# Performance work log

Measured on AMD Instinct MI355X. Metric: run time of the kernel, lower is better.

Reference implementation:

```python
import jax, jax.numpy as jnp
import numpy as np

B, D, H = 32768, 688, 4
DH = D // H          # 172 head dim (d_model // h, overrides ctor d_k)
MH = 128             # mlp hidden
EPS = 1e-5
SCALE = 1.0 / float(np.sqrt(DH))


def _ln(x, g, b):
    m = jnp.mean(x, -1, keepdims=True)
    v = jnp.var(x, -1, keepdims=True)  # biased var, matches torch LayerNorm
    return (x - m) / jnp.sqrt(v + EPS) * g + b


def setup_inputs() -> dict:
    key = jax.random.key(0)
    ks = jax.random.split(key, 16)
    w = lambda k, o, i: jax.random.normal(k, (o, i), jnp.float32) * 0.001  # init.normal_(std=0.001)
    z = lambda n: jnp.zeros((n,), jnp.float32)
    o = lambda n: jnp.ones((n,), jnp.float32)
    return dict(
        x=jax.random.normal(ks[0], (B, D), jnp.float32),
        x2=jax.random.normal(ks[1], (B, D), jnp.float32),
        Wq_v=w(ks[2], D, D), bq_v=z(D),
        Wk_v=w(ks[3], D, D), bk_v=z(D),
        Wv_v=w(ks[4], D, D), bv_v=z(D),
        Wq_i=w(ks[5], D, D), bq_i=z(D),
        Wk_i=w(ks[6], D, D), bk_i=z(D),
        Wv_i=w(ks[7], D, D), bv_i=z(D),
        Wo_v=w(ks[8], D, D), bo_v=z(D),
        Wo_i=w(ks[9], D, D), bo_i=z(D),
        ln1_g=o(D), ln1_b=z(D), ln2_g=o(D), ln2_b=z(D),
        ln3_g=o(D), ln3_b=z(D), ln4_g=o(D), ln4_b=z(D),
        m1v_W=w(ks[10], MH, D), m1v_b=z(MH),
        m2v_W=w(ks[11], D, MH), m2v_b=z(D),
        m1i_W=w(ks[12], MH, D), m1i_b=z(MH),
        m2i_W=w(ks[13], D, MH), m2i_b=z(D),
        coef=o(8),  # LearnableCoefficient 1..8, all init to 1.0
    )


def reference(x, x2,
              Wq_v, bq_v, Wk_v, bk_v, Wv_v, bv_v,
              Wq_i, bq_i, Wk_i, bk_i, Wv_i, bv_i,
              Wo_v, bo_v, Wo_i, bo_i,
              ln1_g, ln1_b, ln2_g, ln2_b, ln3_g, ln3_b, ln4_g, ln4_b,
              m1v_W, m1v_b, m2v_W, m2v_b, m1i_W, m1i_b, m2i_W, m2i_b,
              coef):
    rgb = _ln(x, ln1_g, ln1_b)
    ir = _ln(x2, ln2_g, ln2_b)
    proj = lambda t, W, b: (t @ W.T + b).reshape(-1, H, DH)  # (B, h, d_k)
    q_vis, k_vis, v_vis = proj(rgb, Wq_v, bq_v), proj(rgb, Wk_v, bk_v), proj(rgb, Wv_v, bv_v)
    q_ir, k_ir, v_ir = proj(ir, Wq_i, bq_i), proj(ir, Wk_i, bk_i), proj(ir, Wv_i, bv_i)
    # cross attention over heads: scores are (B, h, h)
    att_vis = jax.nn.softmax(jnp.einsum('bhd,bgd->bhg', q_ir, k_vis) * SCALE, -1)
    att_ir = jax.nn.softmax(jnp.einsum('bhd,bgd->bhg', q_vis, k_ir) * SCALE, -1)
    out_vis = jnp.einsum('bhg,bgd->bhd', att_vis, v_vis).reshape(-1, D) @ Wo_v.T + bo_v
    out_ir = jnp.einsum('bhg,bgd->bhd', att_ir, v_ir).reshape(-1, D) @ Wo_i.T + bo_i
    out_vis = coef[0] * x + coef[1] * out_vis
    out_ir = coef[2] * x2 + coef[3] * out_ir
    mv = jax.nn.gelu(_ln(out_vis, ln3_g, ln3_b) @ m1v_W.T + m1v_b, approximate=False) @ m2v_W.T + m2v_b
    mi = jax.nn.gelu(_ln(out_ir, ln4_g, ln4_b) @ m1i_W.T + m1i_b, approximate=False) @ m2i_W.T + m2i_b
    out_vis = coef[4] * out_vis + coef[5] * mv
    out_ir = coef[6] * out_ir + coef[7] * mi
    return out_vis, out_ir
```

## Files before the change

kernel.cpp:

```cpp
#include <hip/hip_runtime.h>
#include <cmath>


#define B_ROWS 32768
#define D_DIM  688
#define DP     704
#define DH_DIM 172
#define MH_DIM 128

typedef unsigned short ushort_t;
typedef __attribute__((ext_vector_type(8))) __bf16 bf16x8;
typedef __attribute__((ext_vector_type(4))) float  f32x4;

__device__ __forceinline__ float b2f(ushort_t u) {
    return __builtin_bit_cast(float, (unsigned int)u << 16);
}
__device__ __forceinline__ ushort_t f2bf(float f) {
    unsigned int u = __builtin_bit_cast(unsigned int, f);
    u += 0x7FFFu + ((u >> 16) & 1u);
    return (ushort_t)(u >> 16);
}

__device__ __forceinline__ void gl2lds16(const ushort_t* g, ushort_t* l) {
    __builtin_amdgcn_global_load_lds(
        (const __attribute__((address_space(1))) unsigned int*)g,
        (__attribute__((address_space(3))) unsigned int*)l, 16, 0, 0);
}

struct CvtJobs {
    const float* src[12];
    ushort_t*    dst[12];
    int O[12], Opad[12], Kin[12], Kpad[12];
    int bstart[13];
};

__global__ __launch_bounds__(256)
void cvt_all(CvtJobs jobs)
{
    int b = blockIdx.x;
    int j = 0;
    while (b >= jobs.bstart[j + 1]) ++j;
    const int t = (b - jobs.bstart[j]) * 256 + threadIdx.x;
    const int Kpad = jobs.Kpad[j];
    const int Kin  = jobs.Kin[j];
    const int cpr  = Kpad >> 3;
    if (t >= jobs.Opad[j] * cpr) return;
    const int o = t / cpr;
    const int c = t - o * cpr;
    unsigned int p0 = 0, p1 = 0, p2 = 0, p3 = 0;
    if (o < jobs.O[j] && (c * 8 + 8) <= Kin) {
        const float* s = jobs.src[j] + (size_t)o * Kin + c * 8;
        float4 f0 = reinterpret_cast<const float4*>(s)[0];
        float4 f1 = reinterpret_cast<const float4*>(s)[1];
        p0 = f2bf(f0.x) | ((unsigned int)f2bf(f0.y) << 16);
        p1 = f2bf(f0.z) | ((unsigned int)f2bf(f0.w) << 16);
        p2 = f2bf(f1.x) | ((unsigned int)f2bf(f1.y) << 16);
        p3 = f2bf(f1.z) | ((unsigned int)f2bf(f1.w) << 16);
    }
    *reinterpret_cast<uint4*>(jobs.dst[j] + (size_t)o * Kpad + c * 8) =
        make_uint4(p0, p1, p2, p3);
}

__global__ __launch_bounds__(256)
void pack_bias(const float* __restrict__ a0, const float* __restrict__ a1,
               const float* __restrict__ a2, const float* __restrict__ b0,
               const float* __restrict__ b1, const float* __restrict__ b2,
               float* __restrict__ dv, float* __restrict__ di)
{
    int t = blockIdx.x * 256 + threadIdx.x;
    if (t >= 2064) return;
    float v, w;
    if (t < 688)       { v = a0[t];        w = b0[t]; }
    else if (t < 1376) { v = a1[t - 688];  w = b1[t - 688]; }
    else               { v = a2[t - 1376]; w = b2[t - 1376]; }
    dv[t] = v; di[t] = w;
}

__global__ __launch_bounds__(256)
void ln_kernel(const float* __restrict__ Xv, const float* __restrict__ Xi,
               const float* __restrict__ gv, const float* __restrict__ bv,
               const float* __restrict__ gi, const float* __restrict__ bi,
               ushort_t* __restrict__ Yv, ushort_t* __restrict__ Yi)
{
    const int lane = threadIdx.x & 63;
    const int wave = threadIdx.x >> 6;
    const long w = (long)blockIdx.x * 4 + wave;
    const float* X; const float* g; const float* b; ushort_t* Y; long r;
    if (w < B_ROWS) { X = Xv; g = gv; b = bv; Y = Yv; r = w; }
    else            { X = Xi; g = gi; b = bi; Y = Yi; r = w - B_ROWS; }

    const float4* row = reinterpret_cast<const float4*>(X + r * D_DIM);
    float4 v0 = row[lane];
    float4 v1 = row[lane + 64];
    float4 v2 = make_float4(0.f, 0.f, 0.f, 0.f);
    if (lane < 44) v2 = row[lane + 128];

    float s  = v0.x + v0.y + v0.z + v0.w + v1.x + v1.y + v1.z + v1.w
             + v2.x + v2.y + v2.z + v2.w;
    float s2 = v0.x*v0.x + v0.y*v0.y + v0.z*v0.z + v0.w*v0.w
             + v1.x*v1.x + v1.y*v1.y + v1.z*v1.z + v1.w*v1.w
             + v2.x*v2.x + v2.y*v2.y + v2.z*v2.z + v2.w*v2.w;
#pragma unroll
    for (int m = 32; m; m >>= 1) { s += __shfl_xor(s, m); s2 += __shfl_xor(s2, m); }

    const float mean = s * (1.f / 688.f);
    const float var  = s2 * (1.f / 688.f) - mean * mean;
    const float rstd = rsqrtf(var + 1e-5f);

    const float4* g4 = reinterpret_cast<const float4*>(g);
    const float4* b4 = reinterpret_cast<const float4*>(b);
    ushort4* out4 = reinterpret_cast<ushort4*>(Y + r * DP);

    {
        float4 gg = g4[lane], bb = b4[lane];
        ushort4 o;
        o.x = f2bf((v0.x - mean) * rstd * gg.x + bb.x);
        o.y = f2bf((v0.y - mean) * rstd * gg.y + bb.y);
        o.z = f2bf((v0.z - mean) * rstd * gg.z + bb.z);
        o.w = f2bf((v0.w - mean) * rstd * gg.w + bb.w);
        out4[lane] = o;
    }
    {
        float4 gg = g4[lane + 64], bb = b4[lane + 64];
        ushort4 o;
        o.x = f2bf((v1.x - mean) * rstd * gg.x + bb.x);
        o.y = f2bf((v1.y - mean) * rstd * gg.y + bb.y);
        o.z = f2bf((v1.z - mean) * rstd * gg.z + bb.z);
        o.w = f2bf((v1.w - mean) * rstd * gg.w + bb.w);
        out4[lane + 64] = o;
    }
    if (lane < 44) {
        float4 gg = g4[lane + 128], bb = b4[lane + 128];
        ushort4 o;
        o.x = f2bf((v2.x - mean) * rstd * gg.x + bb.x);
        o.y = f2bf((v2.y - mean) * rstd * gg.y + bb.y);
        o.z = f2bf((v2.z - mean) * rstd * gg.z + bb.z);
        o.w = f2bf((v2.w - mean) * rstd * gg.w + bb.w);
        out4[lane + 128] = o;
    } else if (lane < 48) {
        out4[lane + 128] = make_ushort4(0, 0, 0, 0);
    }
}

__global__ __launch_bounds__(256)
void ln_bf16(const ushort_t* __restrict__ Xv, const ushort_t* __restrict__ Xi,
             const float* __restrict__ gv, const float* __restrict__ bv,
             const float* __restrict__ gi, const float* __restrict__ bi,
             ushort_t* __restrict__ Yv, ushort_t* __restrict__ Yi)
{
    const int lane = threadIdx.x & 63;
    const int wave = threadIdx.x >> 6;
    const long w = (long)blockIdx.x * 4 + wave;
    const ushort_t* X; const float* g; const float* b; ushort_t* Y; long r;
    if (w < B_ROWS) { X = Xv; g = gv; b = bv; Y = Yv; r = w; }
    else            { X = Xi; g = gi; b = bi; Y = Yi; r = w - B_ROWS; }

    const ushort4* row = reinterpret_cast<const ushort4*>(X + r * D_DIM);
    ushort4 u0 = row[lane];
    ushort4 u1 = row[lane + 64];
    ushort4 u2 = make_ushort4(0, 0, 0, 0);
    if (lane < 44) u2 = row[lane + 128];

    float f0x = b2f(u0.x), f0y = b2f(u0.y), f0z = b2f(u0.z), f0w = b2f(u0.w);
    float f1x = b2f(u1.x), f1y = b2f(u1.y), f1z = b2f(u1.z), f1w = b2f(u1.w);
    float f2x = b2f(u2.x), f2y = b2f(u2.y), f2z = b2f(u2.z), f2w = b2f(u2.w);

    float s  = f0x + f0y + f0z + f0w + f1x + f1y + f1z + f1w + f2x + f2y + f2z + f2w;
    float s2 = f0x*f0x + f0y*f0y + f0z*f0z + f0w*f0w
             + f1x*f1x + f1y*f1y + f1z*f1z + f1w*f1w
             + f2x*f2x + f2y*f2y + f2z*f2z + f2w*f2w;
#pragma unroll
    for (int m = 32; m; m >>= 1) { s += __shfl_xor(s, m); s2 += __shfl_xor(s2, m); }

    const float mean = s * (1.f / 688.f);
    const float var  = s2 * (1.f / 688.f) - mean * mean;
    const float rstd = rsqrtf(var + 1e-5f);

    const float4* g4 = reinterpret_cast<const float4*>(g);
    const float4* b4 = reinterpret_cast<const float4*>(b);
    ushort4* out4 = reinterpret_cast<ushort4*>(Y + r * DP);

    {
        float4 gg = g4[lane], bb = b4[lane];
        ushort4 o;
        o.x = f2bf((f0x - mean) * rstd * gg.x + bb.x);
        o.y = f2bf((f0y - mean) * rstd * gg.y + bb.y);
        o.z = f2bf((f0z - mean) * rstd * gg.z + bb.z);
        o.w = f2bf((f0w - mean) * rstd * gg.w + bb.w);
        out4[lane] = o;
    }
    {
        float4 gg = g4[lane + 64], bb = b4[lane + 64];
        ushort4 o;
        o.x = f2bf((f1x - mean) * rstd * gg.x + bb.x);
        o.y = f2bf((f1y - mean) * rstd * gg.y + bb.y);
        o.z = f2bf((f1z - mean) * rstd * gg.z + bb.z);
        o.w = f2bf((f1w - mean) * rstd * gg.w + bb.w);
        out4[lane + 64] = o;
    }
    if (lane < 44) {
        float4 gg = g4[lane + 128], bb = b4[lane + 128];
        ushort4 o;
        o.x = f2bf((f2x - mean) * rstd * gg.x + bb.x);
        o.y = f2bf((f2y - mean) * rstd * gg.y + bb.y);
        o.z = f2bf((f2z - mean) * rstd * gg.z + bb.z);
        o.w = f2bf((f2w - mean) * rstd * gg.w + bb.w);
        out4[lane + 128] = o;
    } else if (lane < 48) {
        out4[lane + 128] = make_ushort4(0, 0, 0, 0);
    }
}

template<int MODE>
__global__ __launch_bounds__(256, 4)
void gemm2(const ushort_t* __restrict__ A0, const ushort_t* __restrict__ A1,
           const ushort_t* __restrict__ W0, const ushort_t* __restrict__ W1,
           const float* __restrict__ bias0, const float* __restrict__ bias1,
           void* __restrict__ out0, void* __restrict__ out1,
           const void* __restrict__ res0, const void* __restrict__ res1,
           const float* __restrict__ coef,
           int ca0, int cb0, int ca1, int cb1,
           int NBn, int N, int K, int lda, int ldw, int ldo)
{
    __shared__ __align__(16) ushort_t smem[16384];
    ushort_t* As = smem;
    ushort_t* Bs = smem + 8192;

    const int q  = gridDim.x >> 3;
    const int vb = (blockIdx.x & 7) * q + (blockIdx.x >> 3);
    const int nb = vb % NBn;
    const int tmp = vb / NBn;
    const int mb = tmp & 255;
    const int zz = tmp >> 8;

    const ushort_t* A = zz ? A1 : A0;
    const ushort_t* W = zz ? W1 : W0;
    const float* bias = zz ? bias1 : bias0;
    void* outp        = zz ? out1 : out0;
    const void* resid = zz ? res1 : res0;
    const int ca = zz ? ca1 : ca0;
    const int cb = zz ? cb1 : cb0;

    const int tid  = threadIdx.x;
    const int lane = tid & 63;
    const int wave = tid >> 6;
    const int m0 = mb * 128;
    const int n0 = nb * 128;
    const int wm = (wave >> 1) * 64;
    const int wn = (wave & 1) * 64;

    const int s0 = wave * 128 + lane;
    const int s1 = s0 + 64;
    const ushort_t* pa0 = A + (size_t)(m0 + (s0 >> 2)) * lda + (s0 & 3) * 8;
    const ushort_t* pa1 = A + (size_t)(m0 + (s1 >> 2)) * lda + (s1 & 3) * 8;
    const ushort_t* pb0 = W + (size_t)(n0 + (s0 >> 2)) * ldw + (s0 & 3) * 8;
    const ushort_t* pb1 = W + (size_t)(n0 + (s1 >> 2)) * ldw + (s1 & 3) * 8;

    const f32x4 vzero = {0.f, 0.f, 0.f, 0.f};
    f32x4 acc[4][4];
#pragma unroll
    for (int i = 0; i < 4; ++i)
#pragma unroll
        for (int j = 0; j < 4; ++j)
            acc[i][j] = vzero;

    const int ko = (lane >> 4) * 8;
    const int rl = lane & 15;
    const int nkt = K / 32;

    auto stage = [&](int buf, int kt) {
        const int kof = kt * 32;
        ushort_t* ad = As + buf * 4096 + wave * 1024;
        ushort_t* bd = Bs + buf * 4096 + wave * 1024;
        gl2lds16(pa0 + kof, ad);
        gl2lds16(pa1 + kof, ad + 512);
        gl2lds16(pb0 + kof, bd);
        gl2lds16(pb1 + kof, bd + 512);
    };

    stage(0, 0);
    __syncthreads();

    for (int kt = 0; kt < nkt; ++kt) {
        const int cur = kt & 1;
        if (kt + 1 < nkt) stage(cur ^ 1, kt + 1);

        const ushort_t* Ab = As + cur * 4096;
        const ushort_t* Bb = Bs + cur * 4096;
        bf16x8 af[4], bw[4];
#pragma unroll
        for (int i = 0; i < 4; ++i) {
            af[i] = *reinterpret_cast<const bf16x8*>(&Ab[(wm + i * 16 + rl) * 32 + ko]);
            bw[i] = *reinterpret_cast<const bf16x8*>(&Bb[(wn + i * 16 + rl) * 32 + ko]);
        }
#pragma unroll
        for (int i = 0; i < 4; ++i)
#pragma unroll
            for (int j = 0; j < 4; ++j)
                acc[i][j] = __builtin_amdgcn_mfma_f32_16x16x32_bf16(af[i], bw[j], acc[i][j], 0, 0, 0);
        __syncthreads();
    }

    float cA = 0.f, cB = 1.f;
    if constexpr (MODE == 1 || MODE == 3) { cA = coef[ca]; cB = coef[cb]; }
    const int rb = (lane >> 4) * 4;
    const int cl = lane & 15;
    ushort_t* C = smem;
#pragma unroll
    for (int j = 0; j < 4; ++j) {
        const int lcol = wn + j * 16 + cl;
        const int col = n0 + lcol;
        const float bc = (col < N) ? bias[col] : 0.f;
#pragma unroll
        for (int i = 0; i < 4; ++i) {
            const int lrow = wm + i * 16 + rb;
#pragma unroll
            for (int r = 0; r < 4; ++r) {
                float val = acc[i][j][r] + bc;
                if constexpr (MODE == 2)
                    val = 0.5f * val * (1.0f + erff(val * 0.70710678118654752f));
                C[(lrow + r) * 128 + lcol] = f2bf(val);
            }
        }
    }
    __syncthreads();

#pragma unroll
    for (int p = 0; p < 8; ++p) {
        const int c = tid + p * 256;
        const int lrow = c >> 4;
        const int lcl = (c & 15) * 8;
        const int gcol = n0 + lcl;
        if (gcol >= N) continue;
        const size_t idx = (size_t)(m0 + lrow) * ldo + gcol;
        uint4 pv = *reinterpret_cast<const uint4*>(&C[lrow * 128 + lcl]);
        if constexpr (MODE == 0 || MODE == 2) {
            *reinterpret_cast<uint4*>((ushort_t*)outp + idx) = pv;
        } else if constexpr (MODE == 1) {
            const float* rp = (const float*)resid + idx;
            float4 r0 = reinterpret_cast<const float4*>(rp)[0];
            float4 r1 = reinterpret_cast<const float4*>(rp)[1];
            float rr[8] = {r0.x, r0.y, r0.z, r0.w, r1.x, r1.y, r1.z, r1.w};
            const ushort_t* pu = (const ushort_t*)&pv;
            ushort_t o[8];
#pragma unroll
            for (int k = 0; k < 8; ++k)
                o[k] = f2bf(cA * rr[k] + cB * b2f(pu[k]));
            *reinterpret_cast<uint4*>((ushort_t*)outp + idx) = *reinterpret_cast<uint4*>(o);
        } else {
            uint4 rv = *reinterpret_cast<const uint4*>((const ushort_t*)resid + idx);
            const ushort_t* pu = (const ushort_t*)&pv;
            const ushort_t* ru = (const ushort_t*)&rv;
            float o[8];
#pragma unroll
            for (int k = 0; k < 8; ++k)
                o[k] = cA * b2f(ru[k]) + cB * b2f(pu[k]);
            float4* op = reinterpret_cast<float4*>((float*)outp + idx);
            op[0] = make_float4(o[0], o[1], o[2], o[3]);
            op[1] = make_float4(o[4], o[5], o[6], o[7]);
        }
    }
}

__global__ __launch_bounds__(256)
void attn_kernel(const ushort_t* __restrict__ qkv_v, const ushort_t* __restrict__ qkv_i,
                 ushort_t* __restrict__ ctx_v, ushort_t* __restrict__ ctx_i)
{
    const int lane = threadIdx.x & 63;
    const int wave = threadIdx.x >> 6;
    const long r = (long)blockIdx.x * 4 + wave;
    const ushort_t* bv = qkv_v + r * 2064;
    const ushort_t* bi = qkv_i + r * 2064;

    float sv[4][4], si[4][4];
#pragma unroll
    for (int h = 0; h < 4; ++h)
#pragma unroll
        for (int g = 0; g < 4; ++g) { sv[h][g] = 0.f; si[h][g] = 0.f; }

    float vvr[3][4], vir[3][4];
#pragma unroll
    for (int it = 0; it < 3; ++it) {
        const int d = lane + it * 64;
        const bool ok = d < DH_DIM;
        float qv[4], kv[4], qi[4], ki[4];
#pragma unroll
        for (int h = 0; h < 4; ++h) {
            const int o = h * DH_DIM + d;
            qv[h]      = ok ? b2f(bv[o]) : 0.f;
            kv[h]      = ok ? b2f(bv[D_DIM + o]) : 0.f;
            vvr[it][h] = ok ? b2f(bv[2 * D_DIM + o]) : 0.f;
            qi[h]      = ok ? b2f(bi[o]) : 0.f;
            ki[h]      = ok ? b2f(bi[D_DIM + o]) : 0.f;
            vir[it][h] = ok ? b2f(bi[2 * D_DIM + o]) : 0.f;
        }
#pragma unroll
        for (int h = 0; h < 4; ++h)
#pragma unroll
            for (int g = 0; g < 4; ++g) {
                sv[h][g] += qi[h] * kv[g];
                si[h][g] += qv[h] * ki[g];
            }
    }

#pragma unroll
    for (int h = 0; h < 4; ++h)
#pragma unroll
        for (int g = 0; g < 4; ++g) {
            float a = sv[h][g], b = si[h][g];
#pragma unroll
            for (int m = 32; m; m >>= 1) { a += __shfl_xor(a, m); b += __shfl_xor(b, m); }
            sv[h][g] = a; si[h][g] = b;
        }

    const float scale = 0.07624928516630235f;
    float av[4][4], ai[4][4];
#pragma unroll
    for (int h = 0; h < 4; ++h) {
        float m1 = fmaxf(fmaxf(sv[h][0], sv[h][1]), fmaxf(sv[h][2], sv[h][3])) * scale;
        float m2 = fmaxf(fmaxf(si[h][0], si[h][1]), fmaxf(si[h][2], si[h][3])) * scale;
        float d1 = 0.f, d2 = 0.f;
#pragma unroll
        for (int g = 0; g < 4; ++g) {
            av[h][g] = expf(sv[h][g] * scale - m1); d1 += av[h][g];
            ai[h][g] = expf(si[h][g] * scale - m2); d2 += ai[h][g];
        }
        const float r1 = 1.f / d1, r2 = 1.f / d2;
#pragma unroll
        for (int g = 0; g < 4; ++g) { av[h][g] *= r1; ai[h][g] *= r2; }
    }

#pragma unroll
    for (int it = 0; it < 3; ++it) {
        const int d = lane + it * 64;
        if (d < DH_DIM) {
#pragma unroll
            for (int h = 0; h < 4; ++h) {
                float cv = av[h][0] * vvr[it][0] + av[h][1] * vvr[it][1]
                         + av[h][2] * vvr[it][2] + av[h][3] * vvr[it][3];
                float ci = ai[h][0] * vir[it][0] + ai[h][1] * vir[it][1]
                         + ai[h][2] * vir[it][2] + ai[h][3] * vir[it][3];
                ctx_v[r * DP + h * DH_DIM + d] = f2bf(cv);
                ctx_i[r * DP + h * DH_DIM + d] = f2bf(ci);
            }
        }
    }
    if (lane < 16) {
        ctx_v[r * DP + 688 + lane] = 0;
        ctx_i[r * DP + 688 + lane] = 0;
    }
}

extern "C" void kernel_launch(void* const* d_in, const int* in_sizes, int n_in,
                              void* d_out, int out_size, void* d_ws, size_t ws_size,
                              hipStream_t stream)
{
    if (n_in < 35) return;
    const float* x     = (const float*)d_in[0];
    const float* x2    = (const float*)d_in[1];
    const float* Wq_v  = (const float*)d_in[2];
    const float* bq_v  = (const float*)d_in[3];
    const float* Wk_v  = (const float*)d_in[4];
    const float* bk_v  = (const float*)d_in[5];
    const float* Wv_v  = (const float*)d_in[6];
    const float* bv_v  = (const float*)d_in[7];
    const float* Wq_i  = (const float*)d_in[8];
    const float* bq_i  = (const float*)d_in[9];
    const float* Wk_i  = (const float*)d_in[10];
    const float* bk_i  = (const float*)d_in[11];
    const float* Wv_i  = (const float*)d_in[12];
    const float* bv_i  = (const float*)d_in[13];
    const float* Wo_v  = (const float*)d_in[14];
    const float* bo_v  = (const float*)d_in[15];
    const float* Wo_i  = (const float*)d_in[16];
    const float* bo_i  = (const float*)d_in[17];
    const float* ln1_g = (const float*)d_in[18];
    const float* ln1_b = (const float*)d_in[19];
    const float* ln2_g = (const float*)d_in[20];
    const float* ln2_b = (const float*)d_in[21];
    const float* ln3_g = (const float*)d_in[22];
    const float* ln3_b = (const float*)d_in[23];
    const float* ln4_g = (const float*)d_in[24];
    const float* ln4_b = (const float*)d_in[25];
    const float* m1v_W = (const float*)d_in[26];
    const float* m1v_b = (const float*)d_in[27];
    const float* m2v_W = (const float*)d_in[28];
    const float* m2v_b = (const float*)d_in[29];
    const float* m1i_W = (const float*)d_in[30];
    const float* m1i_b = (const float*)d_in[31];
    const float* m2i_W = (const float*)d_in[32];
    const float* m2i_b = (const float*)d_in[33];
    const float* coef  = (const float*)d_in[34];

    const size_t BDP = (size_t)B_ROWS * DP;
    const size_t BD  = (size_t)B_ROWS * D_DIM;

    char* ws = (char*)d_ws;
    size_t off = 0;
    auto give = [&](size_t bytes) {
        char* p = ws + off;
        off += (bytes + 255) & ~(size_t)255;
        return p;
    };
    ushort_t* Wcat_v = (ushort_t*)give(2176ull * DP * 2);
    ushort_t* Wcat_i = (ushort_t*)give(2176ull * DP * 2);
    ushort_t* Wo_vb  = (ushort_t*)give(768ull * DP * 2);
    ushort_t* Wo_ib  = (ushort_t*)give(768ull * DP * 2);
    ushort_t* m1vb   = (ushort_t*)give(128ull * DP * 2);
    ushort_t* m1ib   = (ushort_t*)give(128ull * DP * 2);
    ushort_t* m2vb   = (ushort_t*)give(768ull * 128 * 2);
    ushort_t* m2ib   = (ushort_t*)give(768ull * 128 * 2);
    float*    bcat_v = (float*)give(2064 * 4);
    float*    bcat_i = (float*)give(2064 * 4);
    char* regX = give(BDP * 2 * 2);
    char* regQ = give((size_t)B_ROWS * 2064 * 2 * 2);
    char* regG = give((size_t)B_ROWS * MH_DIM * 2 * 2);
    if (ws_size < off) return;

    ushort_t* xn_v  = (ushort_t*)regX;
    ushort_t* xn_i  = xn_v + BDP;
    ushort_t* ctx_v = xn_v;
    ushort_t* ctx_i = xn_i;
    ushort_t* h_v   = ctx_v;
    ushort_t* h_i   = ctx_i;
    ushort_t* qkv_v = (ushort_t*)regQ;
    ushort_t* qkv_i = qkv_v + (size_t)B_ROWS * 2064;
    ushort_t* ovb   = (ushort_t*)regQ;
    ushort_t* oib   = ovb + BD;
    ushort_t* g_v   = (ushort_t*)regG;
    ushort_t* g_i   = g_v + (size_t)B_ROWS * MH_DIM;

    float* ov = (float*)d_out;
    float* oi = ov + BD;

    CvtJobs J;
    const float* srcs[12] = {Wq_v, Wk_v, Wv_v, Wq_i, Wk_i, Wv_i,
                             Wo_v, Wo_i, m1v_W, m1i_W, m2v_W, m2i_W};
    ushort_t* dsts[12] = {Wcat_v, Wcat_v + 688 * DP, Wcat_v + 1376 * DP,
                          Wcat_i, Wcat_i + 688 * DP, Wcat_i + 1376 * DP,
                          Wo_vb, Wo_ib, m1vb, m1ib, m2vb, m2ib};
    int Os[12]    = {688, 688, 688, 688, 688, 688, 688, 688, 128, 128, 688, 688};
    int Opads[12] = {688, 688, 800, 688, 688, 800, 768, 768, 128, 128, 768, 768};
    int Kins[12]  = {688, 688, 688, 688, 688, 688, 688, 688, 688, 688, 128, 128};
    int Kpads[12] = {DP, DP, DP, DP, DP, DP, DP, DP, DP, DP, 128, 128};
    int bs = 0;
    for (int j = 0; j < 12; ++j) {
        J.src[j] = srcs[j]; J.dst[j] = dsts[j];
        J.O[j] = Os[j]; J.Opad[j] = Opads[j]; J.Kin[j] = Kins[j]; J.Kpad[j] = Kpads[j];
        J.bstart[j] = bs;
        bs += (Opads[j] * (Kpads[j] >> 3) + 255) / 256;
    }
    J.bstart[12] = bs;
    cvt_all<<<dim3(bs), dim3(256), 0, stream>>>(J);

    pack_bias<<<dim3(9), dim3(256), 0, stream>>>(bq_v, bk_v, bv_v, bq_i, bk_i, bv_i,
                                                 bcat_v, bcat_i);

    ln_kernel<<<dim3(2 * B_ROWS / 4), dim3(256), 0, stream>>>(
        x, x2, ln1_g, ln1_b, ln2_g, ln2_b, xn_v, xn_i);

    gemm2<0><<<dim3(256 * 17 * 2), dim3(256), 0, stream>>>(
        xn_v, xn_i, Wcat_v, Wcat_i, bcat_v, bcat_i, qkv_v, qkv_i,
        nullptr, nullptr, nullptr, 0, 0, 0, 0, 17, 2064, DP, DP, DP, 2064);

    attn_kernel<<<dim3(B_ROWS / 4), dim3(256), 0, stream>>>(qkv_v, qkv_i, ctx_v, ctx_i);

    gemm2<1><<<dim3(256 * 6 * 2), dim3(256), 0, stream>>>(
        ctx_v, ctx_i, Wo_vb, Wo_ib, bo_v, bo_i, ovb, oib,
        x, x2, coef, 0, 1, 2, 3, 6, 688, DP, DP, DP, 688);

    ln_bf16<<<dim3(2 * B_ROWS / 4), dim3(256), 0, stream>>>(
        ovb, oib, ln3_g, ln3_b, ln4_g, ln4_b, h_v, h_i);

    gemm2<2><<<dim3(256 * 1 * 2), dim3(256), 0, stream>>>(
        h_v, h_i, m1vb, m1ib, m1v_b, m1i_b, g_v, g_i,
        nullptr, nullptr, nullptr, 0, 0, 0, 0, 1, 128, DP, DP, DP, 128);

    gemm2<3><<<dim3(256 * 6 * 2), dim3(256), 0, stream>>>(
        g_v, g_i, m2vb, m2ib, m2v_b, m2i_b, ov, oi,
        ovb, oib, coef, 4, 5, 6, 7, 6, 688, 128, 128, 128, 688);
}
```

Baseline: 691.0 us.

## Add 256x256-tile 8-wave GEMM with swizzled LDS and interleaved prefetch for QKV/out-proj

Introduces a new gemm8 kernel that uses 256x256 output tiles with 8 waves, K-step 64, an XOR-swizzled LDS layout, and a staged prefetch of A/B tiles interleaved with MFMA groups and setprio. It replaces gemm2 for the QKV projection and the output projection. To fit the 64-wide K step, the padded K dimension grows from 704 to 768, and the LN/attention zero-fill and weight padding are extended to match. The larger tiles aim to raise operand reuse and MFMA utilization, at the cost of extra padded K work, a full 128KB of LDS per block, and one block per CU.

```diff
diff --git a/kernel.cpp b/kernel.cpp
--- a/kernel.cpp
+++ b/kernel.cpp
@@ -4,7 +4,7 @@
 
 #define B_ROWS 32768
 #define D_DIM  688
-#define DP     704
+#define DP     768
 #define DH_DIM 172
 #define MH_DIM 128
 
@@ -137,7 +137,7 @@
         o.z = f2bf((v2.z - mean) * rstd * gg.z + bb.z);
         o.w = f2bf((v2.w - mean) * rstd * gg.w + bb.w);
         out4[lane + 128] = o;
-    } else if (lane < 48) {
+    } else {
         out4[lane + 128] = make_ushort4(0, 0, 0, 0);
     }
 }
@@ -206,9 +206,195 @@
         o.z = f2bf((f2z - mean) * rstd * gg.z + bb.z);
         o.w = f2bf((f2w - mean) * rstd * gg.w + bb.w);
         out4[lane + 128] = o;
-    } else if (lane < 48) {
+    } else {
         out4[lane + 128] = make_ushort4(0, 0, 0, 0);
     }
+}
+
+template<int MODE>
+__global__ __launch_bounds__(512, 1)
+void gemm8(const ushort_t* __restrict__ A0, const ushort_t* __restrict__ A1,
+           const ushort_t* __restrict__ W0, const ushort_t* __restrict__ W1,
+           const float* __restrict__ bias0, const float* __restrict__ bias1,
+           ushort_t* __restrict__ out0, ushort_t* __restrict__ out1,
+           const float* __restrict__ res0, const float* __restrict__ res1,
+           const float* __restrict__ coef, int ca0, int cb0, int ca1, int cb1,
+           int NBn, int N, int K, int lda, int ldw, int ldo)
+{
+    __shared__ __align__(16) ushort_t lds8[65536];
+
+    const int q8 = gridDim.x >> 3;
+    const int v  = (blockIdx.x & 7) * q8 + (blockIdx.x >> 3);
+    const int nb = v % NBn;
+    const int tmp = v / NBn;
+    const int mb = tmp & 127;
+    const int zz = tmp >> 7;
+
+    const ushort_t* A = zz ? A1 : A0;
+    const ushort_t* W = zz ? W1 : W0;
+    const float* bias = zz ? bias1 : bias0;
+    ushort_t* outp    = zz ? out1 : out0;
+    const float* resid = zz ? res1 : res0;
+    const int ca = zz ? ca1 : ca0;
+    const int cb = zz ? cb1 : cb0;
+
+    const int tid  = threadIdx.x;
+    const int lane = tid & 63;
+    const int wave = tid >> 6;
+    const int wrow = wave >> 2;
+    const int wcol = wave & 3;
+    const int m0 = mb * 256;
+    const int n0 = nb * 256;
+    const int rl16 = lane & 15;
+    const int q4   = lane >> 4;
+
+    const int r0 = tid >> 3;
+    const int u0 = tid & 7;
+    const int swz0 = ((u0 ^ (r0 & 7)) * 8);
+
+    f32x4 acc[8][4];
+#pragma unroll
+    for (int i = 0; i < 8; ++i)
+#pragma unroll
+        for (int j = 0; j < 4; ++j)
+            acc[i][j] = f32x4{0.f, 0.f, 0.f, 0.f};
+
+    const int NT = K >> 6;
+
+#define STAGE8(mat, rbase, ld, kt, hf, tilebase) do {                              \
+    const ushort_t* _s = (mat) + (size_t)((rbase) + (hf)*128 + r0) * (ld)          \
+                         + (kt)*64 + swz0;                                         \
+    gl2lds16(_s,                 (tilebase) + (hf)*8192 + wave*512);               \
+    gl2lds16(_s + 64*(size_t)(ld), (tilebase) + (hf)*8192 + 4096 + wave*512);      \
+} while (0)
+
+#define RD_A(base, mib, kkv) do {                                                  \
+    _Pragma("unroll")                                                              \
+    for (int i = 0; i < 4; ++i) {                                                  \
+        const int row_ = wrow*128 + ((mib)+i)*16 + rl16;                           \
+        const int un_  = (((kkv) >> 3) + q4) ^ (lane & 7);                         \
+        af[i] = *reinterpret_cast<const bf16x8*>((base) + row_*64 + un_*8);        \
+    } } while (0)
+
+#define RD_B(base, kkv) do {                                                       \
+    _Pragma("unroll")                                                              \
+    for (int j = 0; j < 4; ++j) {                                                  \
+        const int row_ = wcol*64 + j*16 + rl16;                                    \
+        const int un_  = (((kkv) >> 3) + q4) ^ (lane & 7);                         \
+        bw[j] = *reinterpret_cast<const bf16x8*>((base) + row_*64 + un_*8);        \
+    } } while (0)
+
+#define MFMA16(mib) do {                                                           \
+    __builtin_amdgcn_s_setprio(1);                                                 \
+    _Pragma("unroll")                                                              \
+    for (int i = 0; i < 4; ++i)                                                    \
+    _Pragma("unroll")                                                              \
+    for (int j = 0; j < 4; ++j)                                                    \
+        acc[(mib)+i][j] =                                                          \
+            __builtin_amdgcn_mfma_f32_16x16x32_bf16(af[i], bw[j], acc[(mib)+i][j], \
+                                                    0, 0, 0);                      \
+    __builtin_amdgcn_s_setprio(0);                                                 \
+} while (0)
+
+    STAGE8(A, m0, lda, 0, 0, lds8);
+    STAGE8(A, m0, lda, 0, 1, lds8);
+    STAGE8(W, n0, ldw, 0, 0, lds8 + 32768);
+    STAGE8(W, n0, ldw, 0, 1, lds8 + 32768);
+    STAGE8(W, n0, ldw, 1, 0, lds8 + 49152);
+    asm volatile("s_waitcnt vmcnt(2)" ::: "memory");
+    __builtin_amdgcn_s_barrier();
+
+    for (int t = 0; t < NT; ++t) {
+        ushort_t* const Ab  = lds8 + ((t & 1) * 16384);
+        ushort_t* const Bb  = lds8 + 32768 + ((t & 1) * 16384);
+        ushort_t* const An  = lds8 + (((t + 1) & 1) * 16384);
+        ushort_t* const Bn1 = lds8 + 32768 + (((t + 1) & 1) * 16384);
+        ushort_t* const Bn2 = Bb;
+        const int tn1 = (t + 1 < NT) ? t + 1 : NT - 1;
+        const int tn2 = (t + 2 < NT) ? t + 2 : NT - 1;
+
+        bf16x8 af[4], bw[4];
+
+        RD_A(Ab, 0, 0);
+        RD_B(Bb, 0);
+        STAGE8(A, m0, lda, tn1, 0, An);
+        STAGE8(W, n0, ldw, tn1, 1, Bn1);
+        __builtin_amdgcn_s_barrier();
+        MFMA16(0);
+        __builtin_amdgcn_s_barrier();
+
+        RD_A(Ab, 4, 0);
+        STAGE8(A, m0, lda, tn1, 1, An);
+        __builtin_amdgcn_s_barrier();
+        MFMA16(4);
+        __builtin_amdgcn_s_barrier();
+
+        RD_A(Ab, 0, 32);
+        RD_B(Bb, 32);
+        __builtin_amdgcn_s_barrier();
+        MFMA16(0);
+        __builtin_amdgcn_s_barrier();
+
+        RD_A(Ab, 4, 32);
+        STAGE8(W, n0, ldw, tn2, 0, Bn2);
+        asm volatile("s_waitcnt vmcnt(2)" ::: "memory");
+        __builtin_amdgcn_s_barrier();
+        MFMA16(4);
+        __builtin_amdgcn_s_barrier();
+    }
+
+    asm volatile("s_waitcnt vmcnt(0)" ::: "memory");
+    __builtin_amdgcn_s_barrier();
+
+    ushort_t* const Cl = lds8;
+#pragma unroll
+    for (int mi = 0; mi < 8; ++mi)
+#pragma unroll
+        for (int nj = 0; nj < 4; ++nj)
+#pragma unroll
+            for (int r = 0; r < 4; ++r) {
+                const int row  = wrow*128 + mi*16 + q4*4 + r;
+                const int colL = wcol*64 + nj*16 + rl16;
+                const int blk  = (colL >> 3) ^ (((row >> 2) & 3) << 1);
+                Cl[row*256 + blk*8 + (colL & 7)] = f2bf(acc[mi][nj][r]);
+            }
+    __syncthreads();
+
+    float cA = 0.f, cB = 1.f;
+    if constexpr (MODE == 1) { cA = coef[ca]; cB = coef[cb]; }
+#pragma unroll
+    for (int it2 = 0; it2 < 16; ++it2) {
+        const int c   = it2 * 512 + tid;
+        const int row = c >> 5;
+        const int lb  = c & 31;
+        const int gcol = n0 + lb * 8;
+        if (gcol >= N) continue;
+        const int pb = lb ^ (((row >> 2) & 3) << 1);
+        uint4 pv = *reinterpret_cast<const uint4*>(Cl + row*256 + pb*8);
+        const ushort_t* pu = (const ushort_t*)&pv;
+        float4 b0 = *reinterpret_cast<const float4*>(bias + gcol);
+        float4 b1 = *reinterpret_cast<const float4*>(bias + gcol + 4);
+        const float bb[8] = {b0.x, b0.y, b0.z, b0.w, b1.x, b1.y, b1.z, b1.w};
+        const size_t idx = (size_t)(m0 + row) * ldo + gcol;
+        ushort_t o[8];
+        if constexpr (MODE == 0) {
+#pragma unroll
+            for (int k = 0; k < 8; ++k) o[k] = f2bf(b2f(pu[k]) + bb[k]);
+        } else {
+            const float* rp = resid + idx;
+            float4 r0_ = reinterpret_cast<const float4*>(rp)[0];
+            float4 r1_ = reinterpret_cast<const float4*>(rp)[1];
+            const float rr[8] = {r0_.x, r0_.y, r0_.z, r0_.w, r1_.x, r1_.y, r1_.z, r1_.w};
+#pragma unroll
+            for (int k = 0; k < 8; ++k)
+                o[k] = f2bf(cA * rr[k] + cB * (b2f(pu[k]) + bb[k]));
+        }
+        *reinterpret_cast<uint4*>(outp + idx) = *reinterpret_cast<uint4*>(o);
+    }
+#undef STAGE8
+#undef RD_A
+#undef RD_B
+#undef MFMA16
 }
 
 template<int MODE>
@@ -256,13 +442,12 @@
     const ushort_t* pb0 = W + (size_t)(n0 + (s0 >> 2)) * ldw + (s0 & 3) * 8;
     const ushort_t* pb1 = W + (size_t)(n0 + (s1 >> 2)) * ldw + (s1 & 3) * 8;
 
-    const f32x4 vzero = {0.f, 0.f, 0.f, 0.f};
     f32x4 acc[4][4];
 #pragma unroll
     for (int i = 0; i < 4; ++i)
 #pragma unroll
         for (int j = 0; j < 4; ++j)
-            acc[i][j] = vzero;
+            acc[i][j] = f32x4{0.f, 0.f, 0.f, 0.f};
 
     const int ko = (lane >> 4) * 8;
     const int rl = lane & 15;
@@ -287,22 +472,22 @@
 
         const ushort_t* Ab = As + cur * 4096;
         const ushort_t* Bb = Bs + cur * 4096;
-        bf16x8 af[4], bw[4];
+        bf16x8 af[4], bwv[4];
 #pragma unroll
         for (int i = 0; i < 4; ++i) {
-            af[i] = *reinterpret_cast<const bf16x8*>(&Ab[(wm + i * 16 + rl) * 32 + ko]);
-            bw[i] = *reinterpret_cast<const bf16x8*>(&Bb[(wn + i * 16 + rl) * 32 + ko]);
+            af[i]  = *reinterpret_cast<const bf16x8*>(&Ab[(wm + i * 16 + rl) * 32 + ko]);
+            bwv[i] = *reinterpret_cast<const bf16x8*>(&Bb[(wn + i * 16 + rl) * 32 + ko]);
         }
 #pragma unroll
         for (int i = 0; i < 4; ++i)
 #pragma unroll
             for (int j = 0; j < 4; ++j)
-                acc[i][j] = __builtin_amdgcn_mfma_f32_16x16x32_bf16(af[i], bw[j], acc[i][j], 0, 0, 0);
+                acc[i][j] = __builtin_amdgcn_mfma_f32_16x16x32_bf16(af[i], bwv[j], acc[i][j], 0, 0, 0);
         __syncthreads();
     }
 
     float cA = 0.f, cB = 1.f;
-    if constexpr (MODE == 1 || MODE == 3) { cA = coef[ca]; cB = coef[cb]; }
+    if constexpr (MODE == 3) { cA = coef[ca]; cB = coef[cb]; }
     const int rb = (lane >> 4) * 4;
     const int cl = lane & 15;
     ushort_t* C = smem;
@@ -334,19 +519,8 @@
         if (gcol >= N) continue;
         const size_t idx = (size_t)(m0 + lrow) * ldo + gcol;
         uint4 pv = *reinterpret_cast<const uint4*>(&C[lrow * 128 + lcl]);
-        if constexpr (MODE == 0 || MODE == 2) {
+        if constexpr (MODE == 2) {
             *reinterpret_cast<uint4*>((ushort_t*)outp + idx) = pv;
-        } else if constexpr (MODE == 1) {
-            const float* rp = (const float*)resid + idx;
-            float4 r0 = reinterpret_cast<const float4*>(rp)[0];
-            float4 r1 = reinterpret_cast<const float4*>(rp)[1];
-            float rr[8] = {r0.x, r0.y, r0.z, r0.w, r1.x, r1.y, r1.z, r1.w};
-            const ushort_t* pu = (const ushort_t*)&pv;
-            ushort_t o[8];
-#pragma unroll
-            for (int k = 0; k < 8; ++k)
-                o[k] = f2bf(cA * rr[k] + cB * b2f(pu[k]));
-            *reinterpret_cast<uint4*>((ushort_t*)outp + idx) = *reinterpret_cast<uint4*>(o);
         } else {
             uint4 rv = *reinterpret_cast<const uint4*>((const ushort_t*)resid + idx);
             const ushort_t* pu = (const ushort_t*)&pv;
@@ -445,9 +619,9 @@
             }
         }
     }
-    if (lane < 16) {
-        ctx_v[r * DP + 688 + lane] = 0;
-        ctx_i[r * DP + 688 + lane] = 0;
+    for (int z = lane; z < 80; z += 64) {
+        ctx_v[r * DP + 688 + z] = 0;
+        ctx_i[r * DP + 688 + z] = 0;
     }
 }
 
@@ -502,8 +676,8 @@
         off += (bytes + 255) & ~(size_t)255;
         return p;
     };
-    ushort_t* Wcat_v = (ushort_t*)give(2176ull * DP * 2);
-    ushort_t* Wcat_i = (ushort_t*)give(2176ull * DP * 2);
+    ushort_t* Wcat_v = (ushort_t*)give(2304ull * DP * 2);
+    ushort_t* Wcat_i = (ushort_t*)give(2304ull * DP * 2);
     ushort_t* Wo_vb  = (ushort_t*)give(768ull * DP * 2);
     ushort_t* Wo_ib  = (ushort_t*)give(768ull * DP * 2);
     ushort_t* m1vb   = (ushort_t*)give(128ull * DP * 2);
@@ -540,7 +714,7 @@
                           Wcat_i, Wcat_i + 688 * DP, Wcat_i + 1376 * DP,
                           Wo_vb, Wo_ib, m1vb, m1ib, m2vb, m2ib};
     int Os[12]    = {688, 688, 688, 688, 688, 688, 688, 688, 128, 128, 688, 688};
-    int Opads[12] = {688, 688, 800, 688, 688, 800, 768, 768, 128, 128, 768, 768};
+    int Opads[12] = {688, 688, 928, 688, 688, 928, 768, 768, 128, 128, 768, 768};
     int Kins[12]  = {688, 688, 688, 688, 688, 688, 688, 688, 688, 688, 128, 128};
     int Kpads[12] = {DP, DP, DP, DP, DP, DP, DP, DP, DP, DP, 128, 128};
     int bs = 0;
@@ -559,15 +733,15 @@
     ln_kernel<<<dim3(2 * B_ROWS / 4), dim3(256), 0, stream>>>(
         x, x2, ln1_g, ln1_b, ln2_g, ln2_b, xn_v, xn_i);
 
-    gemm2<0><<<dim3(256 * 17 * 2), dim3(256), 0, stream>>>(
+    gemm8<0><<<dim3(128 * 9 * 2), dim3(512), 0, stream>>>(
         xn_v, xn_i, Wcat_v, Wcat_i, bcat_v, bcat_i, qkv_v, qkv_i,
-        nullptr, nullptr, nullptr, 0, 0, 0, 0, 17, 2064, DP, DP, DP, 2064);
+        nullptr, nullptr, nullptr, 0, 0, 0, 0, 9, 2064, DP, DP, DP, 2064);
 
     attn_kernel<<<dim3(B_ROWS / 4), dim3(256), 0, stream>>>(qkv_v, qkv_i, ctx_v, ctx_i);
 
-    gemm2<1><<<dim3(256 * 6 * 2), dim3(256), 0, stream>>>(
+    gemm8<1><<<dim3(128 * 3 * 2), dim3(512), 0, stream>>>(
         ctx_v, ctx_i, Wo_vb, Wo_ib, bo_v, bo_i, ovb, oib,
-        x, x2, coef, 0, 1, 2, 3, 6, 688, DP, DP, DP, 688);
+        x, x2, coef, 0, 1, 2, 3, 3, 688, DP, DP, DP, 688);
 
     ln_bf16<<<dim3(2 * B_ROWS / 4), dim3(256), 0, stream>>>(
         ovb, oib, ln3_g, ln3_b, ln4_g, ln4_b, h_v, h_i);
```

Result: no change. 702.0 us (+1.6%).
